# Optimization experiments

Measured on AMD Instinct MI355X. Metric: run time of the kernel, lower is better.

The kernel has to match this reference:

```python
import jax, jax.numpy as jnp
import numpy as np

B, V, L, C, H = 2, 8, 256, 1024, 16

def setup_inputs() -> dict:
    key = jax.random.key(0)
    ks = jax.random.split(key, 6)
    s = 0.02  # init scale for weights
    x = jax.random.normal(ks[0], (B, V, L, C), jnp.float32)
    Wq = jax.random.normal(ks[1], (C, C), jnp.float32) * s
    Wk = jax.random.normal(ks[2], (C, C), jnp.float32) * s
    Wv = jax.random.normal(ks[3], (C, C), jnp.float32) * s
    Wp = jax.random.normal(ks[4], (C, C), jnp.float32) * s
    bp = jnp.zeros((C,), jnp.float32)
    return {"x": x, "Wq": Wq, "Wk": Wk, "Wv": Wv, "Wp": Wp, "bp": bp}

def _view_mask(V, L):
    # view-level allow mask, expanded to token level [S, S]
    vi = jnp.arange(V)
    qv, kv = vi[:, None], vi[None, :]
    cross = ((qv == 0) & (kv == 1)) | ((qv == 1) & (kv == 0))
    later = (qv > 1) | (kv > 1)
    allow = cross | (later & (qv >= kv))  # [V, V]
    return jnp.repeat(jnp.repeat(allow, L, axis=0), L, axis=1)  # [V*L, V*L]

def reference(x, Wq, Wk, Wv, Wp, bp):
    b, v, l, c = x.shape
    h = H
    dh = c // h
    scale = dh ** -0.5
    s = v * l
    xf = x.reshape(b, s, c)
    # torch Linear: y = x @ W.T
    q = (xf @ Wq.T).reshape(b, s, h, dh).transpose(0, 2, 1, 3)  # [b,h,s,dh]
    k = (xf @ Wk.T).reshape(b, s, h, dh).transpose(0, 2, 1, 3)
    vv = (xf @ Wv.T).reshape(b, s, h, dh).transpose(0, 2, 1, 3)
    scores = jnp.einsum('bhqd,bhkd->bhqk', q, k) * scale  # [b,h,s,s]
    mask = _view_mask(v, l)
    scores = jnp.where(mask, scores, -jnp.inf)
    attn = jax.nn.softmax(scores, axis=-1)
    out = jnp.einsum('bhqk,bhkd->bhqd', attn, vv)
    out = out.transpose(0, 2, 1, 3).reshape(b, v, l, c)
    return out @ Wp.T + bp
```

## Files before the change

kernel.cpp:

```cpp
#include <hip/hip_runtime.h>
#include <stdint.h>

typedef unsigned short ushort_t;
typedef __attribute__((ext_vector_type(8))) __bf16 bf16x8;
typedef __attribute__((ext_vector_type(4))) float floatx4;

__device__ __forceinline__ ushort_t f2bf(float f) {
    uint32_t u = __builtin_bit_cast(uint32_t, f);
    u += 0x7fffu + ((u >> 16) & 1u);
    return (ushort_t)(u >> 16);
}

typedef __attribute__((address_space(1))) const void glb_void;
typedef __attribute__((address_space(3))) void lds_void;
__device__ __forceinline__ void gld16(const void* g, void* l) {
    __builtin_amdgcn_global_load_lds((glb_void*)g, (lds_void*)l, 16, 0, 0);
}

#define QSCALE 0.18033688011112042f

__global__ void cast_kernel(const float* __restrict__ x,
                            const float* __restrict__ Wq, const float* __restrict__ Wk,
                            const float* __restrict__ Wv, const float* __restrict__ Wp,
                            ushort_t* __restrict__ xb, ushort_t* __restrict__ Wqkvb,
                            ushort_t* __restrict__ Wpb)
{
    const int64_t NX = 4194304, NW = 1048576;
    int64_t i4 = ((int64_t)blockIdx.x * blockDim.x + threadIdx.x) * 4;
    const float* src; ushort_t* dst; int64_t off;
    if (i4 < NX)            { src = x;  dst = xb;          off = i4; }
    else if (i4 < NX+NW)    { src = Wq; dst = Wqkvb;       off = i4 - NX; }
    else if (i4 < NX+2*NW)  { src = Wk; dst = Wqkvb + NW;  off = i4 - NX - NW; }
    else if (i4 < NX+3*NW)  { src = Wv; dst = Wqkvb + 2*NW;off = i4 - NX - 2*NW; }
    else                    { src = Wp; dst = Wpb;         off = i4 - NX - 3*NW; }
    float4 v = *(const float4*)(src + off);
    ushort4 o;
    o.x = f2bf(v.x); o.y = f2bf(v.y); o.z = f2bf(v.z); o.w = f2bf(v.w);
    *(ushort4*)(dst + off) = o;
}

#define BM 128
#define BK 32

template<int BN_, int MODE>
__global__ __launch_bounds__(256, 3)
void gemm_bt(const ushort_t* __restrict__ A, const ushort_t* __restrict__ Bmat,
             int M, int N, int K,
             ushort_t* __restrict__ qb, ushort_t* __restrict__ kb, ushort_t* __restrict__ vtb,
             float* __restrict__ outf, const float* __restrict__ bias)
{
    constexpr int NB_B = BN_ * BK / 512;
    constexpr int NT   = BN_ / 32;
    constexpr int PER_W = (8 + NB_B) / 4;
    __shared__ ushort_t As[BM * BK];
    __shared__ ushort_t Bs[BN_ * BK];
    const int tid  = threadIdx.x;
    const int lane = tid & 63;
    const int wave = tid >> 6;
    const int m0 = blockIdx.x * BM;
    const int n0 = blockIdx.y * BN_;
    const int wrow = (wave >> 1) * 64;
    const int wcol = (wave & 1) * (BN_ / 2);
    const int q_ = lane >> 4;
    const int ml = lane & 15;

    floatx4 acc[4][NT];
    for (int i = 0; i < 4; i++) for (int j = 0; j < NT; j++) acc[i][j] = floatx4{0.f,0.f,0.f,0.f};

    const int row_l = lane >> 2;
    const int col_l = (lane & 3) * 8;
    const ushort_t* gptr[PER_W]; ushort_t* lptr[PER_W];
    for (int i = 0; i < PER_W; i++) {
        int id = wave * PER_W + i;
        if (id < 8) {
            gptr[i] = A + (int64_t)(m0 + id*16 + row_l) * K + col_l;
            lptr[i] = As + id * 512;
        } else {
            int j = id - 8;
            gptr[i] = Bmat + (int64_t)(n0 + j*16 + row_l) * K + col_l;
            lptr[i] = Bs + j * 512;
        }
    }

    for (int k0 = 0; k0 < K; k0 += BK) {
        __syncthreads();
        for (int i = 0; i < PER_W; i++) gld16(gptr[i] + k0, lptr[i]);
        __syncthreads();
        bf16x8 af[4], bf[NT];
        for (int mt = 0; mt < 4; mt++)
            af[mt] = *(const bf16x8*)(As + (wrow + mt*16 + ml) * BK + q_*8);
        for (int nt = 0; nt < NT; nt++)
            bf[nt] = *(const bf16x8*)(Bs + (wcol + nt*16 + ml) * BK + q_*8);
        for (int mt = 0; mt < 4; mt++)
            for (int nt = 0; nt < NT; nt++)
                acc[mt][nt] = __builtin_amdgcn_mfma_f32_16x16x32_bf16(af[mt], bf[nt], acc[mt][nt], 0, 0, 0);
    }

    if constexpr (MODE == 0) {
        for (int mt = 0; mt < 4; mt++) for (int nt = 0; nt < NT; nt++) {
            floatx4 v = acc[mt][nt];
            int col = n0 + wcol + nt*16 + ml;
            int which = col >> 10;
            int nn = col & 1023;
            int h = nn >> 6, d = nn & 63;
            if (which < 2) {
                ushort_t* dst = (which == 0) ? qb : kb;
                float sc = (which == 0) ? QSCALE : 1.0f;
                for (int r = 0; r < 4; r++) {
                    int rowg = m0 + wrow + mt*16 + q_*4 + r;
                    int b = rowg >> 11, s = rowg & 2047;
                    dst[(((int64_t)(b*16 + h) * 2048 + s) << 6) + d] = f2bf(v[r] * sc);
                }
            } else {
                int rowg0 = m0 + wrow + mt*16 + q_*4;
                int b = rowg0 >> 11, sbase = rowg0 & 2047;
                ushort4 o;
                o.x = f2bf(v[0]); o.y = f2bf(v[1]); o.z = f2bf(v[2]); o.w = f2bf(v[3]);
                *(ushort4*)(vtb + (((int64_t)(b*16 + h) * 64 + d) << 11) + sbase) = o;
            }
        }
    } else {
        for (int mt = 0; mt < 4; mt++) for (int nt = 0; nt < NT; nt++) {
            floatx4 v = acc[mt][nt];
            int col = n0 + wcol + nt*16 + ml;
            float bv = bias[col];
            for (int r = 0; r < 4; r++) {
                int rowg = m0 + wrow + mt*16 + q_*4 + r;
                outf[(int64_t)rowg * N + col] = v[r] + bv;
            }
        }
    }
}

__global__ __launch_bounds__(128, 2)
void attn_kernel(const ushort_t* __restrict__ Q, const ushort_t* __restrict__ Kb,
                 const ushort_t* __restrict__ Vt, ushort_t* __restrict__ Out)
{
    __shared__ ushort_t Kl[8192];
    __shared__ ushort_t Vl[8192];

    int bi = blockIdx.x;
    int xcd = bi & 7;
    int sl  = bi >> 3;
    int bh  = xcd + 8 * (sl & 3);
    int rest = sl >> 2;
    int qv = 7 - (rest >> 2);
    int qt = rest & 3;
    int b = bh >> 4, h = bh & 15;
    int tid = threadIdx.x;
    int wave = tid >> 6, lane = tid & 63;
    int q_ = lane >> 4, ml = lane & 15;
    int s0 = qv*256 + qt*64 + wave*32;

    const ushort_t* Kbh = Kb + ((int64_t)bh << 17);
    const ushort_t* Vbh = Vt + ((int64_t)bh << 17);

    bf16x8 bq[2][2];
    for (int qf = 0; qf < 2; qf++)
        for (int hh = 0; hh < 2; hh++)
            bq[qf][hh] = *(const bf16x8*)(Q + (((int64_t)bh*2048 + s0 + qf*16 + ml) << 6)
                                          + hh*32 + q_*8);

    floatx4 o_acc[2][4];
    for (int qf = 0; qf < 2; qf++) for (int i = 0; i < 4; i++) o_acc[qf][i] = floatx4{0.f,0.f,0.f,0.f};
    float lsum[2] = {0.f, 0.f};

    int views[8]; int nviews;
    if      (qv == 0) { views[0] = 1; nviews = 1; }
    else if (qv == 1) { views[0] = 0; nviews = 1; }
    else { nviews = qv + 1; for (int i = 0; i < nviews; i++) views[i] = i; }

    int m_ = lane & 15, q5 = lane >> 4;
    int kperm = (m_ >> 2)*8 + (m_ & 3);

    for (int vi = 0; vi < nviews; vi++) {
        int kb0 = views[vi] * 256;
        for (int ck = 0; ck < 2; ck++) {
            int koff = kb0 + ck * 128;

            __syncthreads();
            if (wave == 0) {
                #pragma unroll
                for (int id = 0; id < 16; id++) {
                    int w = id >> 2, t = (id >> 1) & 1, hh = id & 1;
                    const ushort_t* g = Kbh
                        + (((int64_t)(koff + w*32 + t*4 + kperm)) << 6) + hh*32 + q5*8;
                    gld16(g, Kl + id*512);
                }
            } else {
                #pragma unroll
                for (int id = 0; id < 16; id++) {
                    int w = id >> 2, dt = id & 3;
                    const ushort_t* g = Vbh
                        + ((int64_t)(dt*16 + m_) << 11) + koff + w*32 + q5*8;
                    gld16(g, Vl + id*512);
                }
            }
            __syncthreads();

            #pragma unroll
            for (int w = 0; w < 4; w++) {
                floatx4 st[2][2];
                #pragma unroll
                for (int t = 0; t < 2; t++) {
                    bf16x8 k0 = *(const bf16x8*)(Kl + (w*4 + t*2 + 0)*512 + lane*8);
                    bf16x8 k1 = *(const bf16x8*)(Kl + (w*4 + t*2 + 1)*512 + lane*8);
                    #pragma unroll
                    for (int qf = 0; qf < 2; qf++) {
                        floatx4 cz = floatx4{0.f,0.f,0.f,0.f};
                        cz = __builtin_amdgcn_mfma_f32_16x16x32_bf16(k0, bq[qf][0], cz, 0, 0, 0);
                        cz = __builtin_amdgcn_mfma_f32_16x16x32_bf16(k1, bq[qf][1], cz, 0, 0, 0);
                        st[t][qf] = cz;
                    }
                }
                bf16x8 pb[2];
                #pragma unroll
                for (int qf = 0; qf < 2; qf++) {
                    union { ushort_t u[8]; bf16x8 v; } pu;
                    #pragma unroll
                    for (int t = 0; t < 2; t++)
                        #pragma unroll
                        for (int r = 0; r < 4; r++) {
                            float p = __builtin_amdgcn_exp2f(st[t][qf][r]);
                            lsum[qf] += p;
                            pu.u[t*4 + r] = f2bf(p);
                        }
                    pb[qf] = pu.v;
                }
                #pragma unroll
                for (int dt = 0; dt < 4; dt++) {
                    bf16x8 vf = *(const bf16x8*)(Vl + (w*4 + dt)*512 + lane*8);
                    #pragma unroll
                    for (int qf = 0; qf < 2; qf++)
                        o_acc[qf][dt] = __builtin_amdgcn_mfma_f32_16x16x32_bf16(vf, pb[qf], o_acc[qf][dt], 0, 0, 0);
                }
            }
        }
    }

    for (int off = 16; off < 64; off <<= 1)
        for (int qf = 0; qf < 2; qf++)
            lsum[qf] += __shfl_xor(lsum[qf], off);

    for (int qf = 0; qf < 2; qf++) {
        float inv = 1.0f / lsum[qf];
        int sr = s0 + qf*16 + ml;
        for (int dt = 0; dt < 4; dt++) {
            ushort4 o;
            o.x = f2bf(o_acc[qf][dt][0] * inv);
            o.y = f2bf(o_acc[qf][dt][1] * inv);
            o.z = f2bf(o_acc[qf][dt][2] * inv);
            o.w = f2bf(o_acc[qf][dt][3] * inv);
            *(ushort4*)(Out + ((int64_t)b*2048 + sr) * 1024 + h*64 + dt*16 + q_*4) = o;
        }
    }
}

extern "C" void kernel_launch(void* const* d_in, const int* in_sizes, int n_in,
                              void* d_out, int out_size, void* d_ws, size_t ws_size,
                              hipStream_t stream) {
    const float* x  = (const float*)d_in[0];
    const float* Wq = (const float*)d_in[1];
    const float* Wk = (const float*)d_in[2];
    const float* Wv = (const float*)d_in[3];
    const float* Wp = (const float*)d_in[4];
    const float* bp = (const float*)d_in[5];
    float* out = (float*)d_out;

    char* ws = (char*)d_ws;
    ushort_t* xb    = (ushort_t*)(ws);
    ushort_t* Wqkvb = (ushort_t*)(ws + ((size_t)8  << 20));
    ushort_t* Wpb   = (ushort_t*)(ws + ((size_t)14 << 20));
    ushort_t* qb    = (ushort_t*)(ws + ((size_t)16 << 20));
    ushort_t* kbuf  = (ushort_t*)(ws + ((size_t)24 << 20));
    ushort_t* vtb   = (ushort_t*)(ws + ((size_t)40 << 20));
    ushort_t* attno = xb;

    cast_kernel<<<8192, 256, 0, stream>>>(x, Wq, Wk, Wv, Wp, xb, Wqkvb, Wpb);

    dim3 g0(4096 / BM, 3072 / 128);
    gemm_bt<128, 0><<<g0, 256, 0, stream>>>(xb, Wqkvb, 4096, 3072, 1024,
                                            qb, kbuf, vtb, nullptr, nullptr);

    attn_kernel<<<1024, 128, 0, stream>>>(qb, kbuf, vtb, attno);

    dim3 g1(4096 / BM, 1024 / 64);
    gemm_bt<64, 1><<<g1, 256, 0, stream>>>(attno, Wpb, 4096, 1024, 1024,
                                           nullptr, nullptr, nullptr, out, bp);
}
```

Baseline: 186.2 us.

## Split attention over key views with atomic fp32 accumulation and finalize pass

Each attention block now handles one (query view, key view) pair instead of looping over all allowed key views, so the grid grows from 1024 to 4480 blocks and the causal imbalance between blocks goes away. Partial outputs and row sums are accumulated into fp32 workspace buffers with atomicAdd. A new finalize kernel normalises and casts the result to bf16. In exchange this adds memsets, many global atomics on a 16 MB buffer, and an extra kernel pass. Because no max is subtracted, it relies on unscaled exp2 being additive across splits.

```diff
diff --git a/kernel.cpp b/kernel.cpp
--- a/kernel.cpp
+++ b/kernel.cpp
@@ -134,23 +134,32 @@
 
 __global__ __launch_bounds__(128, 2)
 void attn_kernel(const ushort_t* __restrict__ Q, const ushort_t* __restrict__ Kb,
-                 const ushort_t* __restrict__ Vt, ushort_t* __restrict__ Out)
+                 const ushort_t* __restrict__ Vt,
+                 float* __restrict__ accO, float* __restrict__ accL)
 {
     __shared__ ushort_t Kl[8192];
     __shared__ ushort_t Vl[8192];
 
     int bi = blockIdx.x;
-    int xcd = bi & 7;
-    int sl  = bi >> 3;
-    int bh  = xcd + 8 * (sl & 3);
-    int rest = sl >> 2;
-    int qv = 7 - (rest >> 2);
-    int qt = rest & 3;
+    int bh  = (bi & 7) + 8 * ((bi >> 3) & 3);
+    int slot = bi >> 5;
+    int qt = slot & 3;
+    int vs = slot >> 2;
+    int qv, view;
+    if      (vs < 8)  { qv = 7; view = vs; }
+    else if (vs < 15) { qv = 6; view = vs - 8; }
+    else if (vs < 21) { qv = 5; view = vs - 15; }
+    else if (vs < 26) { qv = 4; view = vs - 21; }
+    else if (vs < 30) { qv = 3; view = vs - 26; }
+    else if (vs < 33) { qv = 2; view = vs - 30; }
+    else if (vs == 33){ qv = 1; view = 0; }
+    else              { qv = 0; view = 1; }
     int b = bh >> 4, h = bh & 15;
     int tid = threadIdx.x;
     int wave = tid >> 6, lane = tid & 63;
     int q_ = lane >> 4, ml = lane & 15;
     int s0 = qv*256 + qt*64 + wave*32;
+    int kb0 = view * 256;
 
     const ushort_t* Kbh = Kb + ((int64_t)bh << 17);
     const ushort_t* Vbh = Vt + ((int64_t)bh << 17);
@@ -165,95 +174,95 @@
     for (int qf = 0; qf < 2; qf++) for (int i = 0; i < 4; i++) o_acc[qf][i] = floatx4{0.f,0.f,0.f,0.f};
     float lsum[2] = {0.f, 0.f};
 
-    int views[8]; int nviews;
-    if      (qv == 0) { views[0] = 1; nviews = 1; }
-    else if (qv == 1) { views[0] = 0; nviews = 1; }
-    else { nviews = qv + 1; for (int i = 0; i < nviews; i++) views[i] = i; }
-
     int m_ = lane & 15, q5 = lane >> 4;
     int kperm = (m_ >> 2)*8 + (m_ & 3);
 
-    for (int vi = 0; vi < nviews; vi++) {
-        int kb0 = views[vi] * 256;
-        for (int ck = 0; ck < 2; ck++) {
-            int koff = kb0 + ck * 128;
-
-            __syncthreads();
-            if (wave == 0) {
-                #pragma unroll
-                for (int id = 0; id < 16; id++) {
-                    int w = id >> 2, t = (id >> 1) & 1, hh = id & 1;
-                    const ushort_t* g = Kbh
-                        + (((int64_t)(koff + w*32 + t*4 + kperm)) << 6) + hh*32 + q5*8;
-                    gld16(g, Kl + id*512);
-                }
-            } else {
-                #pragma unroll
-                for (int id = 0; id < 16; id++) {
-                    int w = id >> 2, dt = id & 3;
-                    const ushort_t* g = Vbh
-                        + ((int64_t)(dt*16 + m_) << 11) + koff + w*32 + q5*8;
-                    gld16(g, Vl + id*512);
-                }
-            }
-            __syncthreads();
-
-            #pragma unroll
-            for (int w = 0; w < 4; w++) {
-                floatx4 st[2][2];
-                #pragma unroll
-                for (int t = 0; t < 2; t++) {
-                    bf16x8 k0 = *(const bf16x8*)(Kl + (w*4 + t*2 + 0)*512 + lane*8);
-                    bf16x8 k1 = *(const bf16x8*)(Kl + (w*4 + t*2 + 1)*512 + lane*8);
-                    #pragma unroll
-                    for (int qf = 0; qf < 2; qf++) {
-                        floatx4 cz = floatx4{0.f,0.f,0.f,0.f};
-                        cz = __builtin_amdgcn_mfma_f32_16x16x32_bf16(k0, bq[qf][0], cz, 0, 0, 0);
-                        cz = __builtin_amdgcn_mfma_f32_16x16x32_bf16(k1, bq[qf][1], cz, 0, 0, 0);
-                        st[t][qf] = cz;
-                    }
-                }
-                bf16x8 pb[2];
+    for (int ck = 0; ck < 2; ck++) {
+        int koff = kb0 + ck * 128;
+
+        __syncthreads();
+        if (wave == 0) {
+            #pragma unroll
+            for (int id = 0; id < 16; id++) {
+                int w = id >> 2, t = (id >> 1) & 1, hh = id & 1;
+                const ushort_t* g = Kbh
+                    + (((int64_t)(koff + w*32 + t*4 + kperm)) << 6) + hh*32 + q5*8;
+                gld16(g, Kl + id*512);
+            }
+        } else {
+            #pragma unroll
+            for (int id = 0; id < 16; id++) {
+                int w = id >> 2, dt = id & 3;
+                const ushort_t* g = Vbh
+                    + ((int64_t)(dt*16 + m_) << 11) + koff + w*32 + q5*8;
+                gld16(g, Vl + id*512);
+            }
+        }
+        __syncthreads();
+
+        #pragma unroll
+        for (int w = 0; w < 4; w++) {
+            floatx4 st[2][2];
+            #pragma unroll
+            for (int t = 0; t < 2; t++) {
+                bf16x8 k0 = *(const bf16x8*)(Kl + (w*4 + t*2 + 0)*512 + lane*8);
+                bf16x8 k1 = *(const bf16x8*)(Kl + (w*4 + t*2 + 1)*512 + lane*8);
                 #pragma unroll
                 for (int qf = 0; qf < 2; qf++) {
-                    union { ushort_t u[8]; bf16x8 v; } pu;
+                    floatx4 cz = floatx4{0.f,0.f,0.f,0.f};
+                    cz = __builtin_amdgcn_mfma_f32_16x16x32_bf16(k0, bq[qf][0], cz, 0, 0, 0);
+                    cz = __builtin_amdgcn_mfma_f32_16x16x32_bf16(k1, bq[qf][1], cz, 0, 0, 0);
+                    st[t][qf] = cz;
+                }
+            }
+            bf16x8 pb[2];
+            #pragma unroll
+            for (int qf = 0; qf < 2; qf++) {
+                union { ushort_t u[8]; bf16x8 v; } pu;
+                #pragma unroll
+                for (int t = 0; t < 2; t++)
                     #pragma unroll
-                    for (int t = 0; t < 2; t++)
-                        #pragma unroll
-                        for (int r = 0; r < 4; r++) {
-                            float p = __builtin_amdgcn_exp2f(st[t][qf][r]);
-                            lsum[qf] += p;
-                            pu.u[t*4 + r] = f2bf(p);
-                        }
-                    pb[qf] = pu.v;
-                }
+                    for (int r = 0; r < 4; r++) {
+                        float p = __builtin_amdgcn_exp2f(st[t][qf][r]);
+                        lsum[qf] += p;
+                        pu.u[t*4 + r] = f2bf(p);
+                    }
+                pb[qf] = pu.v;
+            }
+            #pragma unroll
+            for (int dt = 0; dt < 4; dt++) {
+                bf16x8 vf = *(const bf16x8*)(Vl + (w*4 + dt)*512 + lane*8);
                 #pragma unroll
-                for (int dt = 0; dt < 4; dt++) {
-                    bf16x8 vf = *(const bf16x8*)(Vl + (w*4 + dt)*512 + lane*8);
-                    #pragma unroll
-                    for (int qf = 0; qf < 2; qf++)
-                        o_acc[qf][dt] = __builtin_amdgcn_mfma_f32_16x16x32_bf16(vf, pb[qf], o_acc[qf][dt], 0, 0, 0);
-                }
-            }
-        }
-    }
-
-    for (int off = 16; off < 64; off <<= 1)
-        for (int qf = 0; qf < 2; qf++)
-            lsum[qf] += __shfl_xor(lsum[qf], off);
+                for (int qf = 0; qf < 2; qf++)
+                    o_acc[qf][dt] = __builtin_amdgcn_mfma_f32_16x16x32_bf16(vf, pb[qf], o_acc[qf][dt], 0, 0, 0);
+            }
+        }
+    }
 
     for (int qf = 0; qf < 2; qf++) {
-        float inv = 1.0f / lsum[qf];
         int sr = s0 + qf*16 + ml;
-        for (int dt = 0; dt < 4; dt++) {
-            ushort4 o;
-            o.x = f2bf(o_acc[qf][dt][0] * inv);
-            o.y = f2bf(o_acc[qf][dt][1] * inv);
-            o.z = f2bf(o_acc[qf][dt][2] * inv);
-            o.w = f2bf(o_acc[qf][dt][3] * inv);
-            *(ushort4*)(Out + ((int64_t)b*2048 + sr) * 1024 + h*64 + dt*16 + q_*4) = o;
-        }
-    }
+        float* rowp = accO + (((int64_t)b*2048 + sr) << 10) + h*64;
+        for (int dt = 0; dt < 4; dt++)
+            for (int r = 0; r < 4; r++)
+                atomicAdd(rowp + dt*16 + q_*4 + r, o_acc[qf][dt][r]);
+        atomicAdd(accL + bh*2048 + sr, lsum[qf]);
+    }
+}
+
+__global__ void attn_finalize(const float* __restrict__ accO, const float* __restrict__ accL,
+                              ushort_t* __restrict__ attno)
+{
+    int t = blockIdx.x * 256 + threadIdx.x;
+    int64_t e = (int64_t)t * 4;
+    int c = (int)(e & 1023);
+    int s = (int)((e >> 10) & 2047);
+    int b = (int)(e >> 21);
+    float inv = 1.0f / accL[(b*16 + (c >> 6))*2048 + s];
+    float4 v = *(const float4*)(accO + e);
+    ushort4 o;
+    o.x = f2bf(v.x * inv); o.y = f2bf(v.y * inv);
+    o.z = f2bf(v.z * inv); o.w = f2bf(v.w * inv);
+    *(ushort4*)(attno + e) = o;
 }
 
 extern "C" void kernel_launch(void* const* d_in, const int* in_sizes, int n_in,
@@ -273,16 +282,23 @@
     ushort_t* Wpb   = (ushort_t*)(ws + ((size_t)14 << 20));
     ushort_t* qb    = (ushort_t*)(ws + ((size_t)16 << 20));
     ushort_t* kbuf  = (ushort_t*)(ws + ((size_t)24 << 20));
+    float*    accL  = (float*)   (ws + ((size_t)32 << 20));
     ushort_t* vtb   = (ushort_t*)(ws + ((size_t)40 << 20));
+    float*    accO  = (float*)   (ws + ((size_t)48 << 20));
     ushort_t* attno = xb;
 
     cast_kernel<<<8192, 256, 0, stream>>>(x, Wq, Wk, Wv, Wp, xb, Wqkvb, Wpb);
+
+    hipMemsetAsync(accO, 0, (size_t)16 << 20, stream);
+    hipMemsetAsync(accL, 0, (size_t)256 << 10, stream);
 
     dim3 g0(4096 / BM, 3072 / 128);
     gemm_bt<128, 0><<<g0, 256, 0, stream>>>(xb, Wqkvb, 4096, 3072, 1024,
                                             qb, kbuf, vtb, nullptr, nullptr);
 
-    attn_kernel<<<1024, 128, 0, stream>>>(qb, kbuf, vtb, attno);
+    attn_kernel<<<4480, 128, 0, stream>>>(qb, kbuf, vtb, accO, accL);
+
+    attn_finalize<<<4096, 256, 0, stream>>>(accO, accL, attno);
 
     dim3 g1(4096 / BM, 1024 / 64);
     gemm_bt<64, 1><<<g1, 256, 0, stream>>>(attno, Wpb, 4096, 1024, 1024,
```

Measured after the change: 424.8 us. 2.28x slower.
